# Kernel optimization log

Measured on AMD Instinct MI355X. Metric: run time of the kernel, lower is better.

## Reference

```python
import jax, jax.numpy as jnp
import numpy as np

D = 1024      # model_dim
DK = 1024     # keys_dim
DV = 1024     # values_dim
H = 16        # heads
HDK = DK // H # per-head key dim (64)
HDV = DV // H
FF = 2048     # FFN default hidden_dim
EPS = 1e-5


def setup_inputs() -> dict:
    key = jax.random.key(0)
    ks = jax.random.split(key, 16)
    s = lambda k, sh, fan: jax.random.normal(k, sh, jnp.float32) * (1.0 / np.sqrt(fan))
    return {
        "x": jax.random.normal(ks[0], (8, 1024, D), jnp.float32),
        # per-head projections stored as [D, H, hd] (concat of the H small Linears)
        "Wq": s(ks[1], (D, H, HDK), D), "bq": jnp.zeros((H, HDK), jnp.float32),
        "Wk": s(ks[2], (D, H, HDK), D), "bk": jnp.zeros((H, HDK), jnp.float32),
        "Wv": s(ks[3], (D, H, HDV), D), "bv": jnp.zeros((H, HDV), jnp.float32),
        "Wo": s(ks[4], (DV, D), DV), "bo": jnp.zeros((D,), jnp.float32),
        "ln1_g": jnp.ones((D,), jnp.float32), "ln1_b": jnp.zeros((D,), jnp.float32),
        "W1": s(ks[5], (D, FF), D), "b1": jnp.zeros((FF,), jnp.float32),
        "W2": s(ks[6], (FF, D), FF), "b2": jnp.zeros((D,), jnp.float32),
        "ln2_g": jnp.ones((D,), jnp.float32), "ln2_b": jnp.zeros((D,), jnp.float32),
    }


def layer_norm(x, g, b):
    mu = jnp.mean(x, axis=-1, keepdims=True)
    var = jnp.mean(jnp.square(x - mu), axis=-1, keepdims=True)
    return (x - mu) * jax.lax.rsqrt(var + EPS) * g + b


def reference(x, Wq, bq, Wk, bk, Wv, bv, Wo, bo, ln1_g, ln1_b, W1, b1, W2, b2, ln2_g, ln2_b):
    # per-head projections (equivalent to H small Linears, batched)
    q = jnp.einsum("bsd,dhk->bhsk", x, Wq) + bq[:, None, :]
    k = jnp.einsum("bsd,dhk->bhsk", x, Wk) + bk[:, None, :]
    v = jnp.einsum("bsd,dhv->bhsv", x, Wv) + bv[:, None, :]
    # scaled dot-product attention per head (scale uses per-head dk)
    scores = jnp.einsum("bhsk,bhtk->bhst", q, k) / jnp.sqrt(jnp.float32(HDK))
    w = jax.nn.softmax(scores, axis=-1)
    ctx = jnp.einsum("bhst,bhtv->bhsv", w, v)           # [B,H,S,hdv]
    B, _, S, _ = ctx.shape
    ctx = ctx.transpose(0, 2, 1, 3).reshape(B, S, DV)   # concat heads
    c = ctx @ Wo + bo
    h = layer_norm(x + c, ln1_g, ln1_b)
    y = jax.nn.relu(h @ W1 + b1) @ W2 + b2
    return layer_norm(h + y, ln2_g, ln2_b)
```

## Files before the change

### kernel.cpp

```cpp
#include <hip/hip_runtime.h>
#include <hip/hip_bf16.h>
#include <cstdint>

typedef __bf16 bf16_t;
typedef __bf16 bf16x8 __attribute__((ext_vector_type(8)));
typedef __bf16 bf16x4 __attribute__((ext_vector_type(4)));
typedef float f32x4 __attribute__((ext_vector_type(4)));

#define SEQ    1024
#define BATCH  8
#define NTOK   8192
#define DMODEL 1024
#define NHEAD  16
#define HD     64
#define FFDIM  2048

__device__ __forceinline__ void async16(const void* g, void* l) {
  __builtin_amdgcn_global_load_lds(
      (const __attribute__((address_space(1))) void*)g,
      (__attribute__((address_space(3))) void*)l, 16, 0, 0);
}

__global__ __launch_bounds__(256)
void cast_bf16_kernel(const float* __restrict__ in, bf16_t* __restrict__ out, int n4) {
  int i = blockIdx.x * 256 + threadIdx.x;
  if (i >= n4) return;
  float4 v = ((const float4*)in)[i];
  bf16x4 o = { (bf16_t)v.x, (bf16_t)v.y, (bf16_t)v.z, (bf16_t)v.w };
  *(bf16x4*)&out[(size_t)i * 4] = o;
}

__global__ __launch_bounds__(256)
void transpose_cast_kernel(const float* __restrict__ W, bf16_t* __restrict__ Wt,
                           int R, int C) {
  __shared__ float tile[32][33];
  const int bx = blockIdx.x * 32;
  const int by = blockIdx.y * 32;
  const int tx = threadIdx.x;
  const int ty = threadIdx.y;
#pragma unroll
  for (int i = 0; i < 4; ++i)
    tile[ty + 8 * i][tx] = W[(size_t)(by + ty + 8 * i) * C + bx + tx];
  __syncthreads();
#pragma unroll
  for (int i = 0; i < 4; ++i)
    Wt[(size_t)(bx + ty + 8 * i) * R + by + tx] = (bf16_t)tile[tx][ty + 8 * i];
}

template <int EPI>
__global__ __launch_bounds__(256)
void gemm_bt(const bf16_t* __restrict__ A, const bf16_t* __restrict__ Bt,
             const float* __restrict__ bias, void* __restrict__ outp,
             int M, int N, int K, float scale) {
  __shared__ bf16_t As[128 * 64];
  __shared__ bf16_t Bs[128 * 64];
  const int tid = threadIdx.x;
  const int wave = tid >> 6, lane = tid & 63;
  const int wr = (wave >> 1) * 64, wc = (wave & 1) * 64;
  const int bm = blockIdx.x * 128, bn = blockIdx.y * 128;

  f32x4 acc[4][4];
#pragma unroll
  for (int i = 0; i < 4; ++i)
#pragma unroll
    for (int j = 0; j < 4; ++j) acc[i][j] = (f32x4){0.f, 0.f, 0.f, 0.f};

  const int lcol = (lane & 7) * 8;
  const int fr = lane & 15, kg = (lane >> 4) * 8;

  const int nk = K >> 6;
  for (int kt = 0; kt < nk; ++kt) {
    const int k0 = kt << 6;
#pragma unroll
    for (int i = 0; i < 4; ++i) {
      const int chunk = i * 4 + wave;
      const int row = chunk * 8 + (lane >> 3);
      async16(&A[(size_t)(bm + row) * K + k0 + lcol], &As[chunk * 512]);
      async16(&Bt[(size_t)(bn + row) * K + k0 + lcol], &Bs[chunk * 512]);
    }
    asm volatile("s_waitcnt vmcnt(0)" ::: "memory");
    __syncthreads();

#pragma unroll
    for (int kk = 0; kk < 2; ++kk) {
      bf16x8 a[4], b[4];
      const int ko = kk * 32 + kg;
#pragma unroll
      for (int i = 0; i < 4; ++i) a[i] = *(const bf16x8*)&As[(wr + i * 16 + fr) * 64 + ko];
#pragma unroll
      for (int j = 0; j < 4; ++j) b[j] = *(const bf16x8*)&Bs[(wc + j * 16 + fr) * 64 + ko];
#pragma unroll
      for (int i = 0; i < 4; ++i)
#pragma unroll
        for (int j = 0; j < 4; ++j)
          acc[i][j] = __builtin_amdgcn_mfma_f32_16x16x32_bf16(a[i], b[j], acc[i][j], 0, 0, 0);
    }
    __syncthreads();
  }

  const int lr = (lane >> 4) * 4, lc = lane & 15;
#pragma unroll
  for (int j = 0; j < 4; ++j) {
    const int col = bn + wc + j * 16 + lc;
    const float bv = bias[col];
#pragma unroll
    for (int i = 0; i < 4; ++i) {
#pragma unroll
      for (int r = 0; r < 4; ++r) {
        const int row = bm + wr + i * 16 + lr + r;
        const float v = (acc[i][j][r] + bv) * scale;
        if (EPI == 0) {
          ((float*)outp)[(size_t)row * N + col] = v;
        } else if (EPI == 1) {
          ((bf16_t*)outp)[(size_t)row * N + col] = (bf16_t)fmaxf(v, 0.f);
        } else if (EPI == 2) {
          const int b_ = row >> 10, s_ = row & 1023, h_ = col >> 6, e_ = col & 63;
          ((bf16_t*)outp)[((size_t)((b_ * NHEAD + h_) * SEQ + s_)) * HD + e_] = (bf16_t)v;
        } else {
          const int b_ = row >> 10, s_ = row & 1023, h_ = col >> 6, e_ = col & 63;
          ((bf16_t*)outp)[((size_t)((b_ * NHEAD + h_) * HD + e_)) * SEQ + s_] = (bf16_t)v;
        }
      }
    }
  }
}

__global__ __launch_bounds__(256)
void attn_kernel(const bf16_t* __restrict__ Q, const bf16_t* __restrict__ K,
                 const bf16_t* __restrict__ VT, bf16_t* __restrict__ CTX) {
  const int bh = blockIdx.x;
  const int qt = blockIdx.y * 128;
  const int b_ = bh >> 4, h_ = bh & 15;
  const bf16_t* qh = Q + (size_t)bh * SEQ * HD;
  const bf16_t* kh = K + (size_t)bh * SEQ * HD;
  const bf16_t* vh = VT + (size_t)bh * HD * SEQ;
  const int tid = threadIdx.x, wave = tid >> 6, lane = tid & 63;
  const int fr = lane & 15, kg = (lane >> 4) * 8;
  const int lr = (lane >> 4) * 4, lc = lane & 15;

  __shared__ bf16_t Ks[2][64 * 64];
  __shared__ bf16_t Vs[2][64 * 64];
  __shared__ bf16_t Ps[128 * 64];

  const int srow = lane >> 3;
  const int scol = ((lane & 7) ^ srow) * 8;

  bf16x8 qf[2][2];
#pragma unroll
  for (int i = 0; i < 2; ++i)
#pragma unroll
    for (int kk = 0; kk < 2; ++kk)
      qf[i][kk] = *(const bf16x8*)&qh[(size_t)(qt + wave * 32 + i * 16 + fr) * HD + kk * 32 + kg];

  f32x4 octx[2][4];
  float mrun[2][4], lrun[2][4];
#pragma unroll
  for (int i = 0; i < 2; ++i)
#pragma unroll
    for (int j = 0; j < 4; ++j) octx[i][j] = (f32x4){0.f, 0.f, 0.f, 0.f};
#pragma unroll
  for (int i = 0; i < 2; ++i)
#pragma unroll
    for (int r = 0; r < 4; ++r) { mrun[i][r] = -1e30f; lrun[i][r] = 0.f; }

  auto stage = [&](int buf, int t) {
#pragma unroll
    for (int i = 0; i < 2; ++i) {
      const int ch = i * 4 + wave;
      const int row = ch * 8 + srow;
      async16(&kh[(size_t)(t * 64 + row) * HD + scol], &Ks[buf][ch * 512]);
      async16(&vh[(size_t)row * SEQ + t * 64 + scol], &Vs[buf][ch * 512]);
    }
  };

  stage(0, 0);
  asm volatile("s_waitcnt vmcnt(0)" ::: "memory");
  __syncthreads();

  for (int t = 0; t < SEQ / 64; ++t) {
    const int cur = t & 1;
    if (t + 1 < SEQ / 64) stage(cur ^ 1, t + 1);

    f32x4 sc[2][4];
#pragma unroll
    for (int i = 0; i < 2; ++i)
#pragma unroll
      for (int j = 0; j < 4; ++j) sc[i][j] = (f32x4){0.f, 0.f, 0.f, 0.f};
#pragma unroll
    for (int kk = 0; kk < 2; ++kk) {
      bf16x8 kf[4];
#pragma unroll
      for (int j = 0; j < 4; ++j) {
        const int row = j * 16 + fr;
        kf[j] = *(const bf16x8*)&Ks[cur][row * 64 + ((kk * 32 + kg) ^ ((row & 7) << 3))];
      }
#pragma unroll
      for (int i = 0; i < 2; ++i)
#pragma unroll
        for (int j = 0; j < 4; ++j)
          sc[i][j] = __builtin_amdgcn_mfma_f32_16x16x32_bf16(qf[i][kk], kf[j], sc[i][j], 0, 0, 0);
    }

    float pmx[2][4];
    int ok = 1;
#pragma unroll
    for (int i = 0; i < 2; ++i)
#pragma unroll
      for (int r = 0; r < 4; ++r) {
        const float m3 = fmaxf(fmaxf(sc[i][0][r], sc[i][1][r]),
                               fmaxf(sc[i][2][r], sc[i][3][r]));
        pmx[i][r] = m3;
        ok &= (m3 <= mrun[i][r] + 8.f) ? 1 : 0;
      }
    if (!__all(ok)) {
#pragma unroll
      for (int i = 0; i < 2; ++i)
#pragma unroll
        for (int r = 0; r < 4; ++r) {
          float mx = pmx[i][r];
#pragma unroll
          for (int m = 1; m < 16; m <<= 1) mx = fmaxf(mx, __shfl_xor(mx, m));
          const float mnew = fmaxf(mrun[i][r], mx);
          const float alpha = exp2f(mrun[i][r] - mnew);
          mrun[i][r] = mnew;
          lrun[i][r] *= alpha;
#pragma unroll
          for (int j = 0; j < 4; ++j) octx[i][j][r] *= alpha;
        }
    }
#pragma unroll
    for (int i = 0; i < 2; ++i)
#pragma unroll
      for (int r = 0; r < 4; ++r) {
        const float m = mrun[i][r];
        float s = 0.f;
#pragma unroll
        for (int j = 0; j < 4; ++j) {
          const float p = exp2f(sc[i][j][r] - m);
          sc[i][j][r] = p;
          s += p;
        }
        lrun[i][r] += s;
        const int prow = wave * 32 + i * 16 + lr + r;
#pragma unroll
        for (int j = 0; j < 4; ++j)
          Ps[prow * 64 + (((j * 16 + lc)) ^ ((prow & 7) << 3))] = (bf16_t)sc[i][j][r];
      }
    asm volatile("s_waitcnt lgkmcnt(0)" ::: "memory");

#pragma unroll
    for (int kk = 0; kk < 2; ++kk) {
      bf16x8 pf[2], vf[4];
#pragma unroll
      for (int i = 0; i < 2; ++i) {
        const int row = wave * 32 + i * 16 + fr;
        pf[i] = *(const bf16x8*)&Ps[row * 64 + ((kk * 32 + kg) ^ ((row & 7) << 3))];
      }
#pragma unroll
      for (int j = 0; j < 4; ++j) {
        const int row = j * 16 + fr;
        vf[j] = *(const bf16x8*)&Vs[cur][row * 64 + ((kk * 32 + kg) ^ ((row & 7) << 3))];
      }
#pragma unroll
      for (int i = 0; i < 2; ++i)
#pragma unroll
        for (int j = 0; j < 4; ++j)
          octx[i][j] = __builtin_amdgcn_mfma_f32_16x16x32_bf16(pf[i], vf[j], octx[i][j], 0, 0, 0);
    }

    asm volatile("s_waitcnt vmcnt(0)" ::: "memory");
    __syncthreads();
  }

#pragma unroll
  for (int i = 0; i < 2; ++i)
#pragma unroll
    for (int r = 0; r < 4; ++r) {
      float l = lrun[i][r];
#pragma unroll
      for (int m = 1; m < 16; m <<= 1) l += __shfl_xor(l, m);
      const float inv = 1.f / l;
      const int row = qt + wave * 32 + i * 16 + lr + r;
#pragma unroll
      for (int j = 0; j < 4; ++j) {
        const int c = j * 16 + lc;
        CTX[((size_t)(b_ * SEQ + row)) * DMODEL + h_ * HD + c] = (bf16_t)(octx[i][j][r] * inv);
      }
    }
}

__global__ __launch_bounds__(256)
void ln_kernel(const float* __restrict__ X, const float* __restrict__ Y,
               const float* __restrict__ g, const float* __restrict__ b,
               float* __restrict__ outf, bf16_t* __restrict__ outb) {
  const int row = blockIdx.x, tid = threadIdx.x;
  const int wave = tid >> 6, lane = tid & 63;
  const float4 xv = ((const float4*)X)[(size_t)row * 256 + tid];
  const float4 yv = ((const float4*)Y)[(size_t)row * 256 + tid];
  const float s0 = xv.x + yv.x, s1 = xv.y + yv.y, s2 = xv.z + yv.z, s3 = xv.w + yv.w;
  float sum = s0 + s1 + s2 + s3;
  float sq = s0 * s0 + s1 * s1 + s2 * s2 + s3 * s3;
#pragma unroll
  for (int off = 1; off < 64; off <<= 1) {
    sum += __shfl_xor(sum, off);
    sq += __shfl_xor(sq, off);
  }
  __shared__ float red[8];
  if (lane == 0) { red[wave] = sum; red[4 + wave] = sq; }
  __syncthreads();
  sum = red[0] + red[1] + red[2] + red[3];
  sq = red[4] + red[5] + red[6] + red[7];
  const float mu = sum * (1.f / 1024.f);
  const float var = sq * (1.f / 1024.f) - mu * mu;
  const float rstd = rsqrtf(var + 1e-5f);
  const float4 gv = ((const float4*)g)[tid];
  const float4 bv = ((const float4*)b)[tid];
  const float o0 = (s0 - mu) * rstd * gv.x + bv.x;
  const float o1 = (s1 - mu) * rstd * gv.y + bv.y;
  const float o2 = (s2 - mu) * rstd * gv.z + bv.z;
  const float o3 = (s3 - mu) * rstd * gv.w + bv.w;
  ((float4*)outf)[(size_t)row * 256 + tid] = make_float4(o0, o1, o2, o3);
  if (outb) {
    bf16x4 ob = { (bf16_t)o0, (bf16_t)o1, (bf16_t)o2, (bf16_t)o3 };
    *(bf16x4*)&outb[(size_t)row * 1024 + tid * 4] = ob;
  }
}

extern "C" void kernel_launch(void* const* d_in, const int* in_sizes, int n_in,
                              void* d_out, int out_size, void* d_ws, size_t ws_size,
                              hipStream_t stream) {
  const float* x   = (const float*)d_in[0];
  const float* Wq  = (const float*)d_in[1];
  const float* bq  = (const float*)d_in[2];
  const float* Wk  = (const float*)d_in[3];
  const float* bk  = (const float*)d_in[4];
  const float* Wv  = (const float*)d_in[5];
  const float* bv  = (const float*)d_in[6];
  const float* Wo  = (const float*)d_in[7];
  const float* bo  = (const float*)d_in[8];
  const float* g1  = (const float*)d_in[9];
  const float* be1 = (const float*)d_in[10];
  const float* W1  = (const float*)d_in[11];
  const float* b1  = (const float*)d_in[12];
  const float* W2  = (const float*)d_in[13];
  const float* b2  = (const float*)d_in[14];
  const float* g2  = (const float*)d_in[15];
  const float* be2 = (const float*)d_in[16];

  char* ws = (char*)d_ws;
  size_t off = 0;
  auto alloc = [&](size_t bytes) {
    char* p = ws + off;
    off += (bytes + 255) & ~(size_t)255;
    return p;
  };
  const size_t MB = 1u << 20;
  bf16_t* xb  = (bf16_t*)alloc(16 * MB);
  bf16_t* WqT = (bf16_t*)alloc(2 * MB);
  bf16_t* WkT = (bf16_t*)alloc(2 * MB);
  bf16_t* WvT = (bf16_t*)alloc(2 * MB);
  bf16_t* WoT = (bf16_t*)alloc(2 * MB);
  bf16_t* W1T = (bf16_t*)alloc(4 * MB);
  bf16_t* W2T = (bf16_t*)alloc(4 * MB);
  bf16_t* qb  = (bf16_t*)alloc(16 * MB);
  bf16_t* kb  = (bf16_t*)alloc(16 * MB);
  bf16_t* vT  = (bf16_t*)alloc(16 * MB);
  float*  attnf = (float*)alloc(32 * MB);
  float*  h     = (float*)alloc(32 * MB);
  bf16_t* ctx = xb;
  bf16_t* hb  = qb;
  bf16_t* u   = kb;
  float*  y   = attnf;

  cast_bf16_kernel<<<dim3(NTOK * DMODEL / 4 / 256), dim3(256), 0, stream>>>(x, xb, NTOK * DMODEL / 4);
  transpose_cast_kernel<<<dim3(32, 32), dim3(32, 8), 0, stream>>>(Wq, WqT, 1024, 1024);
  transpose_cast_kernel<<<dim3(32, 32), dim3(32, 8), 0, stream>>>(Wk, WkT, 1024, 1024);
  transpose_cast_kernel<<<dim3(32, 32), dim3(32, 8), 0, stream>>>(Wv, WvT, 1024, 1024);
  transpose_cast_kernel<<<dim3(32, 32), dim3(32, 8), 0, stream>>>(Wo, WoT, 1024, 1024);
  transpose_cast_kernel<<<dim3(64, 32), dim3(32, 8), 0, stream>>>(W1, W1T, 1024, 2048);
  transpose_cast_kernel<<<dim3(32, 64), dim3(32, 8), 0, stream>>>(W2, W2T, 2048, 1024);

  const float qscale = 0.125f * 1.44269504088896f;
  gemm_bt<2><<<dim3(64, 8), dim3(256), 0, stream>>>(xb, WqT, bq, qb, NTOK, DMODEL, DMODEL, qscale);
  gemm_bt<2><<<dim3(64, 8), dim3(256), 0, stream>>>(xb, WkT, bk, kb, NTOK, DMODEL, DMODEL, 1.0f);
  gemm_bt<3><<<dim3(64, 8), dim3(256), 0, stream>>>(xb, WvT, bv, vT, NTOK, DMODEL, DMODEL, 1.0f);

  attn_kernel<<<dim3(128, 8), dim3(256), 0, stream>>>(qb, kb, vT, ctx);

  gemm_bt<0><<<dim3(64, 8), dim3(256), 0, stream>>>(ctx, WoT, bo, attnf, NTOK, DMODEL, DMODEL, 1.0f);
  ln_kernel<<<dim3(NTOK), dim3(256), 0, stream>>>(x, attnf, g1, be1, h, hb);

  gemm_bt<1><<<dim3(64, 16), dim3(256), 0, stream>>>(hb, W1T, b1, u, NTOK, FFDIM, DMODEL, 1.0f);
  gemm_bt<0><<<dim3(64, 8), dim3(256), 0, stream>>>(u, W2T, b2, y, NTOK, DMODEL, FFDIM, 1.0f);
  ln_kernel<<<dim3(NTOK), dim3(256), 0, stream>>>(h, y, g2, be2, (float*)d_out, nullptr);
}
```

Baseline: 370.6 us.

## Fuse QKV GEMMs, remap workgroups, use fragment-ordered LDS, drop fp32 LN1 output

The three Q/K/V projection GEMMs become one launch over a concatenated transposed weight, with the epilogue choosing the destination by column range. GEMM workgroups are remapped across 8 groups for better cache locality, and the LDS tiles are loaded in MFMA-fragment order so each lane reads one contiguous 16-byte slot. LN1 now writes only a bf16 result and LN2 reads that bf16 residual, removing an fp32 intermediate and its traffic. The cost is that the second residual is taken from the bf16-rounded h, which lowers precision.

Measured after the change: 456.6 us. +23.2%, slower.

```diff
diff --git a/kernel.cpp b/kernel.cpp
--- a/kernel.cpp
+++ b/kernel.cpp
@@ -50,14 +50,31 @@
 template <int EPI>
 __global__ __launch_bounds__(256)
 void gemm_bt(const bf16_t* __restrict__ A, const bf16_t* __restrict__ Bt,
-             const float* __restrict__ bias, void* __restrict__ outp,
-             int M, int N, int K, float scale) {
-  __shared__ bf16_t As[128 * 64];
-  __shared__ bf16_t Bs[128 * 64];
-  const int tid = threadIdx.x;
-  const int wave = tid >> 6, lane = tid & 63;
-  const int wr = (wave >> 1) * 64, wc = (wave & 1) * 64;
-  const int bm = blockIdx.x * 128, bn = blockIdx.y * 128;
+             const float* __restrict__ bias0, const float* __restrict__ bias1,
+             const float* __restrict__ bias2,
+             void* __restrict__ o0, void* __restrict__ o1, void* __restrict__ o2,
+             int K, int nTN, int ldo, float qscale) {
+  __shared__ bf16_t As[8192];
+  __shared__ bf16_t Bs[8192];
+  const int tid = threadIdx.x, w = tid >> 6, l = tid & 63;
+  const int fr = l & 15, ks = l >> 4;
+
+  const int nwg = gridDim.x, bid = blockIdx.x;
+  const int wg = (bid & 7) * (nwg >> 3) + (bid >> 3);
+  const int tm = wg / nTN, tn = wg - tm * nTN;
+  const int bm = tm << 7, bn = tn << 7;
+
+  const int wr = (w >> 1) * 64, wc = (w & 1) * 64;
+  const int rtA = wr >> 4, rtB = wc >> 4;
+
+  size_t goff[4];
+  int lsub[4];
+#pragma unroll
+  for (int j = 0; j < 4; ++j) {
+    const int sub = w * 4 + j, rt = sub >> 1, ct = sub & 1;
+    goff[j] = (size_t)(rt * 16 + fr) * K + ct * 32 + ks * 8;
+    lsub[j] = sub * 512;
+  }
 
   f32x4 acc[4][4];
 #pragma unroll
@@ -65,18 +82,16 @@
 #pragma unroll
     for (int j = 0; j < 4; ++j) acc[i][j] = (f32x4){0.f, 0.f, 0.f, 0.f};
 
-  const int lcol = (lane & 7) * 8;
-  const int fr = lane & 15, kg = (lane >> 4) * 8;
+  const bf16_t* Ab = A + (size_t)bm * K;
+  const bf16_t* Bb = Bt + (size_t)bn * K;
 
   const int nk = K >> 6;
   for (int kt = 0; kt < nk; ++kt) {
     const int k0 = kt << 6;
 #pragma unroll
-    for (int i = 0; i < 4; ++i) {
-      const int chunk = i * 4 + wave;
-      const int row = chunk * 8 + (lane >> 3);
-      async16(&A[(size_t)(bm + row) * K + k0 + lcol], &As[chunk * 512]);
-      async16(&Bt[(size_t)(bn + row) * K + k0 + lcol], &Bs[chunk * 512]);
+    for (int j = 0; j < 4; ++j) {
+      async16(Ab + k0 + goff[j], &As[lsub[j]]);
+      async16(Bb + k0 + goff[j], &Bs[lsub[j]]);
     }
     asm volatile("s_waitcnt vmcnt(0)" ::: "memory");
     __syncthreads();
@@ -84,11 +99,12 @@
 #pragma unroll
     for (int kk = 0; kk < 2; ++kk) {
       bf16x8 a[4], b[4];
-      const int ko = kk * 32 + kg;
-#pragma unroll
-      for (int i = 0; i < 4; ++i) a[i] = *(const bf16x8*)&As[(wr + i * 16 + fr) * 64 + ko];
-#pragma unroll
-      for (int j = 0; j < 4; ++j) b[j] = *(const bf16x8*)&Bs[(wc + j * 16 + fr) * 64 + ko];
+#pragma unroll
+      for (int i = 0; i < 4; ++i)
+        a[i] = *(const bf16x8*)&As[((rtA + i) * 2 + kk) * 512 + l * 8];
+#pragma unroll
+      for (int j = 0; j < 4; ++j)
+        b[j] = *(const bf16x8*)&Bs[((rtB + j) * 2 + kk) * 512 + l * 8];
 #pragma unroll
       for (int i = 0; i < 4; ++i)
 #pragma unroll
@@ -98,27 +114,33 @@
     __syncthreads();
   }
 
-  const int lr = (lane >> 4) * 4, lc = lane & 15;
+  const int lr = ks * 4, lc = fr;
 #pragma unroll
   for (int j = 0; j < 4; ++j) {
     const int col = bn + wc + j * 16 + lc;
-    const float bv = bias[col];
 #pragma unroll
     for (int i = 0; i < 4; ++i) {
 #pragma unroll
       for (int r = 0; r < 4; ++r) {
         const int row = bm + wr + i * 16 + lr + r;
-        const float v = (acc[i][j][r] + bv) * scale;
+        const float v = acc[i][j][r];
         if (EPI == 0) {
-          ((float*)outp)[(size_t)row * N + col] = v;
+          ((float*)o0)[(size_t)row * ldo + col] = v + bias0[col];
         } else if (EPI == 1) {
-          ((bf16_t*)outp)[(size_t)row * N + col] = (bf16_t)fmaxf(v, 0.f);
-        } else if (EPI == 2) {
-          const int b_ = row >> 10, s_ = row & 1023, h_ = col >> 6, e_ = col & 63;
-          ((bf16_t*)outp)[((size_t)((b_ * NHEAD + h_) * SEQ + s_)) * HD + e_] = (bf16_t)v;
+          ((bf16_t*)o0)[(size_t)row * ldo + col] = (bf16_t)fmaxf(v + bias0[col], 0.f);
         } else {
-          const int b_ = row >> 10, s_ = row & 1023, h_ = col >> 6, e_ = col & 63;
-          ((bf16_t*)outp)[((size_t)((b_ * NHEAD + h_) * HD + e_)) * SEQ + s_] = (bf16_t)v;
+          const int mode = col >> 10, cl = col & 1023;
+          const int b_ = row >> 10, s_ = row & 1023, h_ = cl >> 6, e_ = cl & 63;
+          if (mode == 0) {
+            ((bf16_t*)o0)[((size_t)((b_ * NHEAD + h_) * SEQ + s_)) * HD + e_] =
+                (bf16_t)((v + bias0[cl]) * qscale);
+          } else if (mode == 1) {
+            ((bf16_t*)o1)[((size_t)((b_ * NHEAD + h_) * SEQ + s_)) * HD + e_] =
+                (bf16_t)(v + bias1[cl]);
+          } else {
+            ((bf16_t*)o2)[((size_t)((b_ * NHEAD + h_) * HD + e_)) * SEQ + s_] =
+                (bf16_t)(v + bias2[cl]);
+          }
         }
       }
     }
@@ -276,10 +298,10 @@
   for (int i = 0; i < 2; ++i)
 #pragma unroll
     for (int r = 0; r < 4; ++r) {
-      float l = lrun[i][r];
-#pragma unroll
-      for (int m = 1; m < 16; m <<= 1) l += __shfl_xor(l, m);
-      const float inv = 1.f / l;
+      float lsum = lrun[i][r];
+#pragma unroll
+      for (int m = 1; m < 16; m <<= 1) lsum += __shfl_xor(lsum, m);
+      const float inv = 1.f / lsum;
       const int row = qt + wave * 32 + i * 16 + lr + r;
 #pragma unroll
       for (int j = 0; j < 4; ++j) {
@@ -290,13 +312,13 @@
 }
 
 __global__ __launch_bounds__(256)
-void ln_kernel(const float* __restrict__ X, const float* __restrict__ Y,
-               const float* __restrict__ g, const float* __restrict__ b,
-               float* __restrict__ outf, bf16_t* __restrict__ outb) {
+void ln1_kernel(const float* __restrict__ X, const float* __restrict__ Y0,
+                const float* __restrict__ g, const float* __restrict__ b,
+                bf16_t* __restrict__ outb) {
   const int row = blockIdx.x, tid = threadIdx.x;
   const int wave = tid >> 6, lane = tid & 63;
   const float4 xv = ((const float4*)X)[(size_t)row * 256 + tid];
-  const float4 yv = ((const float4*)Y)[(size_t)row * 256 + tid];
+  const float4 yv = ((const float4*)Y0)[(size_t)row * 256 + tid];
   const float s0 = xv.x + yv.x, s1 = xv.y + yv.y, s2 = xv.z + yv.z, s3 = xv.w + yv.w;
   float sum = s0 + s1 + s2 + s3;
   float sq = s0 * s0 + s1 * s1 + s2 * s2 + s3 * s3;
@@ -315,15 +337,43 @@
   const float rstd = rsqrtf(var + 1e-5f);
   const float4 gv = ((const float4*)g)[tid];
   const float4 bv = ((const float4*)b)[tid];
-  const float o0 = (s0 - mu) * rstd * gv.x + bv.x;
-  const float o1 = (s1 - mu) * rstd * gv.y + bv.y;
-  const float o2 = (s2 - mu) * rstd * gv.z + bv.z;
-  const float o3 = (s3 - mu) * rstd * gv.w + bv.w;
-  ((float4*)outf)[(size_t)row * 256 + tid] = make_float4(o0, o1, o2, o3);
-  if (outb) {
-    bf16x4 ob = { (bf16_t)o0, (bf16_t)o1, (bf16_t)o2, (bf16_t)o3 };
-    *(bf16x4*)&outb[(size_t)row * 1024 + tid * 4] = ob;
-  }
+  bf16x4 ob = { (bf16_t)((s0 - mu) * rstd * gv.x + bv.x),
+                (bf16_t)((s1 - mu) * rstd * gv.y + bv.y),
+                (bf16_t)((s2 - mu) * rstd * gv.z + bv.z),
+                (bf16_t)((s3 - mu) * rstd * gv.w + bv.w) };
+  *(bf16x4*)&outb[(size_t)row * 1024 + tid * 4] = ob;
+}
+
+__global__ __launch_bounds__(256)
+void ln2_kernel(const bf16_t* __restrict__ Hb, const float* __restrict__ Y0,
+                const float* __restrict__ g, const float* __restrict__ b,
+                float* __restrict__ outf) {
+  const int row = blockIdx.x, tid = threadIdx.x;
+  const int wave = tid >> 6, lane = tid & 63;
+  const bf16x4 hv = *(const bf16x4*)&Hb[(size_t)row * 1024 + tid * 4];
+  const float4 y0 = ((const float4*)Y0)[(size_t)row * 256 + tid];
+  const float s0 = (float)hv[0] + y0.x, s1 = (float)hv[1] + y0.y;
+  const float s2 = (float)hv[2] + y0.z, s3 = (float)hv[3] + y0.w;
+  float sum = s0 + s1 + s2 + s3;
+  float sq = s0 * s0 + s1 * s1 + s2 * s2 + s3 * s3;
+#pragma unroll
+  for (int off = 1; off < 64; off <<= 1) {
+    sum += __shfl_xor(sum, off);
+    sq += __shfl_xor(sq, off);
+  }
+  __shared__ float red[8];
+  if (lane == 0) { red[wave] = sum; red[4 + wave] = sq; }
+  __syncthreads();
+  sum = red[0] + red[1] + red[2] + red[3];
+  sq = red[4] + red[5] + red[6] + red[7];
+  const float mu = sum * (1.f / 1024.f);
+  const float var = sq * (1.f / 1024.f) - mu * mu;
+  const float rstd = rsqrtf(var + 1e-5f);
+  const float4 gv = ((const float4*)g)[tid];
+  const float4 bv = ((const float4*)b)[tid];
+  ((float4*)outf)[(size_t)row * 256 + tid] =
+      make_float4((s0 - mu) * rstd * gv.x + bv.x, (s1 - mu) * rstd * gv.y + bv.y,
+                  (s2 - mu) * rstd * gv.z + bv.z, (s3 - mu) * rstd * gv.w + bv.w);
 }
 
 extern "C" void kernel_launch(void* const* d_in, const int* in_sizes, int n_in,
@@ -348,49 +398,45 @@
   const float* be2 = (const float*)d_in[16];
 
   char* ws = (char*)d_ws;
-  size_t off = 0;
-  auto alloc = [&](size_t bytes) {
-    char* p = ws + off;
-    off += (bytes + 255) & ~(size_t)255;
-    return p;
-  };
   const size_t MB = 1u << 20;
-  bf16_t* xb  = (bf16_t*)alloc(16 * MB);
-  bf16_t* WqT = (bf16_t*)alloc(2 * MB);
-  bf16_t* WkT = (bf16_t*)alloc(2 * MB);
-  bf16_t* WvT = (bf16_t*)alloc(2 * MB);
-  bf16_t* WoT = (bf16_t*)alloc(2 * MB);
-  bf16_t* W1T = (bf16_t*)alloc(4 * MB);
-  bf16_t* W2T = (bf16_t*)alloc(4 * MB);
-  bf16_t* qb  = (bf16_t*)alloc(16 * MB);
-  bf16_t* kb  = (bf16_t*)alloc(16 * MB);
-  bf16_t* vT  = (bf16_t*)alloc(16 * MB);
-  float*  attnf = (float*)alloc(32 * MB);
-  float*  h     = (float*)alloc(32 * MB);
+  bf16_t* xb    = (bf16_t*)(ws + 0 * MB);
+  bf16_t* WqkvT = (bf16_t*)(ws + 16 * MB);
+  bf16_t* WoT   = (bf16_t*)(ws + 22 * MB);
+  bf16_t* W1T   = (bf16_t*)(ws + 24 * MB);
+  bf16_t* W2T   = (bf16_t*)(ws + 28 * MB);
+  bf16_t* qb    = (bf16_t*)(ws + 32 * MB);
+  bf16_t* kb    = (bf16_t*)(ws + 48 * MB);
+  bf16_t* vT    = (bf16_t*)(ws + 64 * MB);
+  float*  y0    = (float*)(ws + 80 * MB);
   bf16_t* ctx = xb;
   bf16_t* hb  = qb;
   bf16_t* u   = kb;
-  float*  y   = attnf;
 
   cast_bf16_kernel<<<dim3(NTOK * DMODEL / 4 / 256), dim3(256), 0, stream>>>(x, xb, NTOK * DMODEL / 4);
-  transpose_cast_kernel<<<dim3(32, 32), dim3(32, 8), 0, stream>>>(Wq, WqT, 1024, 1024);
-  transpose_cast_kernel<<<dim3(32, 32), dim3(32, 8), 0, stream>>>(Wk, WkT, 1024, 1024);
-  transpose_cast_kernel<<<dim3(32, 32), dim3(32, 8), 0, stream>>>(Wv, WvT, 1024, 1024);
+  transpose_cast_kernel<<<dim3(32, 32), dim3(32, 8), 0, stream>>>(Wq, WqkvT, 1024, 1024);
+  transpose_cast_kernel<<<dim3(32, 32), dim3(32, 8), 0, stream>>>(Wk, WqkvT + 1024 * 1024, 1024, 1024);
+  transpose_cast_kernel<<<dim3(32, 32), dim3(32, 8), 0, stream>>>(Wv, WqkvT + 2 * 1024 * 1024, 1024, 1024);
   transpose_cast_kernel<<<dim3(32, 32), dim3(32, 8), 0, stream>>>(Wo, WoT, 1024, 1024);
   transpose_cast_kernel<<<dim3(64, 32), dim3(32, 8), 0, stream>>>(W1, W1T, 1024, 2048);
   transpose_cast_kernel<<<dim3(32, 64), dim3(32, 8), 0, stream>>>(W2, W2T, 2048, 1024);
 
   const float qscale = 0.125f * 1.44269504088896f;
-  gemm_bt<2><<<dim3(64, 8), dim3(256), 0, stream>>>(xb, WqT, bq, qb, NTOK, DMODEL, DMODEL, qscale);
-  gemm_bt<2><<<dim3(64, 8), dim3(256), 0, stream>>>(xb, WkT, bk, kb, NTOK, DMODEL, DMODEL, 1.0f);
-  gemm_bt<3><<<dim3(64, 8), dim3(256), 0, stream>>>(xb, WvT, bv, vT, NTOK, DMODEL, DMODEL, 1.0f);
+
+  gemm_bt<2><<<dim3(1536), dim3(256), 0, stream>>>(
+      xb, WqkvT, bq, bk, bv, qb, kb, vT, 1024, 24, 0, qscale);
 
   attn_kernel<<<dim3(128, 8), dim3(256), 0, stream>>>(qb, kb, vT, ctx);
 
-  gemm_bt<0><<<dim3(64, 8), dim3(256), 0, stream>>>(ctx, WoT, bo, attnf, NTOK, DMODEL, DMODEL, 1.0f);
-  ln_kernel<<<dim3(NTOK), dim3(256), 0, stream>>>(x, attnf, g1, be1, h, hb);
-
-  gemm_bt<1><<<dim3(64, 16), dim3(256), 0, stream>>>(hb, W1T, b1, u, NTOK, FFDIM, DMODEL, 1.0f);
-  gemm_bt<0><<<dim3(64, 8), dim3(256), 0, stream>>>(u, W2T, b2, y, NTOK, DMODEL, FFDIM, 1.0f);
-  ln_kernel<<<dim3(NTOK), dim3(256), 0, stream>>>(h, y, g2, be2, (float*)d_out, nullptr);
-}
+  gemm_bt<0><<<dim3(512), dim3(256), 0, stream>>>(
+      ctx, WoT, bo, nullptr, nullptr, y0, nullptr, nullptr, 1024, 8, 1024, 1.f);
+
+  ln1_kernel<<<dim3(NTOK), dim3(256), 0, stream>>>(x, y0, g1, be1, hb);
+
+  gemm_bt<1><<<dim3(1024), dim3(256), 0, stream>>>(
+      hb, W1T, b1, nullptr, nullptr, u, nullptr, nullptr, 1024, 16, 2048, 1.f);
+
+  gemm_bt<0><<<dim3(512), dim3(256), 0, stream>>>(
+      u, W2T, b2, nullptr, nullptr, y0, nullptr, nullptr, 2048, 8, 1024, 1.f);
+
+  ln2_kernel<<<dim3(NTOK), dim3(256), 0, stream>>>(hb, y0, g2, be2, (float*)d_out);
+}
```
